# Kernel optimization log

Hardware: AMD Instinct MI355X
Metric: run time of the kernel (lower is better)

The kernel has to match this reference:

```python
import jax, jax.numpy as jnp
import numpy as np

B, S, NE = 4096, 128, 2
H = 64  # lstm hidden

def setup_inputs() -> dict:
    key = jax.random.key(0)
    ks = jax.random.split(key, 12)
    d = {
        'self_obs':     jax.random.normal(ks[0], (B, S, 15), jnp.float32),
        'teammate_obs': jax.random.normal(ks[1], (B, S, 13), jnp.float32),
        'enemy_obs':    jax.random.normal(ks[2], (B, S, NE, 13), jnp.float32),
        'next_cp_obs':  jax.random.normal(ks[3], (B, S, 6), jnp.float32),
        'W1':  jax.random.normal(ks[4], (47, 256), jnp.float32) * 0.1,
        'b1':  jnp.zeros((256,), jnp.float32),
        'W2':  jax.random.normal(ks[5], (256, 128), jnp.float32) * 0.1,
        'b2':  jnp.zeros((128,), jnp.float32),
        'Wih': jax.random.normal(ks[6], (128, 4 * H), jnp.float32) * 0.1,
        'bih': jnp.zeros((4 * H,), jnp.float32),
        'Whh': jax.random.normal(ks[7], (H, 4 * H), jnp.float32) * 0.1,
        'bhh': jnp.zeros((4 * H,), jnp.float32),
        'Wv':  jax.random.normal(ks[8], (H, 1), jnp.float32) * 0.1,
        'bv':  jnp.zeros((1,), jnp.float32),
    }
    return d

def reference(self_obs, teammate_obs, enemy_obs, next_cp_obs,
              W1, b1, W2, b2, Wih, bih, Whh, bhh, Wv, bv):
    # enemy pooling + concat -> [B,S,47]
    en_mean = enemy_obs.mean(axis=2)
    x = jnp.concatenate([self_obs, teammate_obs, en_mean, next_cp_obs], axis=2)
    # MLP encoder -> [B,S,128]
    emb = jax.nn.relu(jax.nn.relu(x @ W1 + b1) @ W2 + b2)
    # precompute input projection for all timesteps -> [B,S,4H]
    wx = emb @ Wih + bih
    h0 = jnp.zeros((B, H), wx.dtype)
    c0 = jnp.zeros((B, H), wx.dtype)

    def step(carry, wx_t):
        h, c = carry
        gates = wx_t + h @ Whh + bhh          # [B,4H]
        i, f, g, o = jnp.split(gates, 4, axis=-1)
        i = jax.nn.sigmoid(i)
        f = jax.nn.sigmoid(f)
        g = jnp.tanh(g)
        o = jax.nn.sigmoid(o)
        c = f * c + i * g
        h = o * jnp.tanh(c)
        return (h, c), h

    (hn, cn), outs = jax.lax.scan(step, (h0, c0), jnp.swapaxes(wx, 0, 1))
    out = jnp.swapaxes(outs, 0, 1)            # [B,S,H]
    val = (out @ Wv + bv).reshape(B, S, 1)
    return val, hn[None], cn[None]
```

## Files before the change

### kernel.cpp

```cpp
#include <hip/hip_runtime.h>
#include <hip/hip_bf16.h>

#define BB 4096
#define SS 128
#define NB 16
#define NT 256

typedef __attribute__((ext_vector_type(8))) short short8;
typedef __attribute__((ext_vector_type(4))) float f32x4;
typedef unsigned short ushort_t;
typedef unsigned int uint_t;

#define SX_STR   72
#define SH1_STR  264
#define SEMB_STR 136
#define SH_STR   72
#define ENC_LDS_USHORTS (64 * SH1_STR + 64 * SEMB_STR)

__device__ __forceinline__ ushort_t f2bf(float f) {
    union { __hip_bfloat16 b; ushort_t u; } x;
    x.b = __float2bfloat16(f);
    return x.u;
}
__device__ __forceinline__ uint_t pack2(float a, float b) {
    return (uint_t)f2bf(a) | ((uint_t)f2bf(b) << 16);
}
__device__ __forceinline__ float bflo(uint_t u) {
    union { unsigned u; float f; } x; x.u = u << 16; return x.f;
}
__device__ __forceinline__ float bfhi(uint_t u) {
    union { unsigned u; float f; } x; x.u = u & 0xFFFF0000u; return x.f;
}
__device__ __forceinline__ float bf2f(ushort_t h) {
    union { unsigned u; float f; } x; x.u = ((unsigned)h) << 16; return x.f;
}
__device__ __forceinline__ float fsig(float x) {
    return __builtin_amdgcn_rcpf(1.f + __expf(-x));
}
__device__ __forceinline__ float ftanh(float x) {
    return 1.f - 2.f * __builtin_amdgcn_rcpf(__expf(2.f * x) + 1.f);
}
__device__ __forceinline__ void barrier_lgkm() {
    asm volatile("s_waitcnt lgkmcnt(0)\n\ts_barrier" ::: "memory");
}

union FragU { short8 v; ushort_t u[8]; };

__global__ void podcritic_prep(const float* __restrict__ W1, const float* __restrict__ W2,
                               const float* __restrict__ Wih, const float* __restrict__ Whh,
                               short8* __restrict__ img)
{
    const int W = blockIdx.x * 4 + (threadIdx.x >> 6);
    const int l = threadIdx.x & 63;
    const int q = l >> 4, m = l & 15;
    FragU u;
    #pragma unroll
    for (int j = 0; j < 8; ++j) {
        float v;
        if (W < 32)       { int nt = W >> 1,        kk = W & 1;        int k = kk*32 + q*8 + j;
                            v = (k < 47) ? W1[k*256 + nt*16 + m] : 0.f; }
        else if (W < 96)  { int f = W - 32, nt = f >> 3, kk = f & 7;   int k = kk*32 + q*8 + j;
                            v = W2[k*128 + nt*16 + m]; }
        else if (W < 160) { int f = W - 96, nt = f >> 2, kk = f & 3;   int k = kk*32 + q*8 + j;
                            v = Wih[k*256 + nt*16 + m]; }
        else              { int f = W - 160, nt = f >> 1, kk = f & 1;  int k = kk*32 + q*8 + j;
                            v = Whh[k*256 + nt*16 + m]; }
        u.u[j] = f2bf(v);
    }
    img[W * 64 + l] = u.v;
}

__device__ __forceinline__ void enc_block(
    ushort_t* smem,
    const float* __restrict__ self_obs, const float* __restrict__ tm_obs,
    const float* __restrict__ en_obs,   const float* __restrict__ cp_obs,
    const float* __restrict__ b1, const float* __restrict__ b2,
    const float* __restrict__ bih, const float* __restrict__ bhh,
    const short8* __restrict__ img, uint_t* __restrict__ wx, int c0, int e)
{
    ushort_t* sh1 = smem;
    ushort_t* sxe = smem + 64 * SH1_STR;

    const int t = threadIdx.x;
    const int w = t >> 6, l = t & 63, q = l >> 4, m = l & 15;
    const int bg = e & 255, b0 = bg * NB;
    const int ytile = e >> 8;
    const int sbase = c0 + ytile * 4;

    {
        const int col = t & 63, rw0 = t >> 6;
        const float* p; int stride, soff; float scale;
        if (col < 15)      { p = self_obs + col;      stride = 15; soff = 0;  scale = 0.5f; }
        else if (col < 28) { p = tm_obs + (col - 15); stride = 13; soff = 0;  scale = 0.5f; }
        else if (col < 41) { p = en_obs + (col - 28); stride = 26; soff = 13; scale = 0.5f; }
        else if (col < 47) { p = cp_obs + (col - 41); stride = 6;  soff = 0;  scale = 0.5f; }
        else               { p = self_obs;            stride = 0;  soff = 0;  scale = 0.f; }
        #pragma unroll
        for (int jj = 0; jj < 16; ++jj) {
            int rr = 4 * jj + rw0;
            int mt = rr >> 4, r = rr & 15;
            int bs = (b0 + r) * SS + sbase + mt;
            int o = bs * stride;
            float v = scale * (p[o] + p[o + soff]);
            sxe[rr * SX_STR + col] = f2bf(v);
        }
    }
    float bias1[4], bias2[2], bgf[4];
    #pragma unroll
    for (int i = 0; i < 4; ++i) bias1[i] = b1[w * 64 + i * 16 + m];
    #pragma unroll
    for (int i = 0; i < 2; ++i) bias2[i] = b2[32 * w + 16 * i + m];
    #pragma unroll
    for (int i = 0; i < 4; ++i) { int n = (w + 4 * i) * 16 + m; bgf[i] = bih[n] + bhh[n]; }
    barrier_lgkm();

    {
        short8 w1f[4][2];
        #pragma unroll
        for (int i = 0; i < 4; ++i)
            #pragma unroll
            for (int kk = 0; kk < 2; ++kk)
                w1f[i][kk] = img[(((4 * w + i) * 2) + kk) * 64 + l];
        f32x4 c1[4][4];
        #pragma unroll
        for (int mt = 0; mt < 4; ++mt)
            #pragma unroll
            for (int i = 0; i < 4; ++i)
                c1[mt][i] = (f32x4){bias1[i], bias1[i], bias1[i], bias1[i]};
        #pragma unroll
        for (int kk = 0; kk < 2; ++kk) {
            #pragma unroll
            for (int mt = 0; mt < 4; ++mt) {
                short8 a = *(const short8*)&sxe[(mt * 16 + m) * SX_STR + kk * 32 + q * 8];
                #pragma unroll
                for (int i = 0; i < 4; ++i)
                    c1[mt][i] = __builtin_amdgcn_mfma_f32_16x16x32_bf16(a, w1f[i][kk], c1[mt][i], 0, 0, 0);
            }
        }
        #pragma unroll
        for (int mt = 0; mt < 4; ++mt)
            #pragma unroll
            for (int i = 0; i < 4; ++i) {
                int col = w * 64 + i * 16 + m;
                #pragma unroll
                for (int r = 0; r < 4; ++r)
                    sh1[(mt * 16 + q * 4 + r) * SH1_STR + col] = f2bf(fmaxf(c1[mt][i][r], 0.f));
            }
    }
    barrier_lgkm();

    {
        short8 w2f[2][8];
        #pragma unroll
        for (int i = 0; i < 2; ++i)
            #pragma unroll
            for (int kk = 0; kk < 8; ++kk)
                w2f[i][kk] = img[(32 + ((2 * w + i) * 8) + kk) * 64 + l];
        f32x4 c2[4][2];
        #pragma unroll
        for (int mt = 0; mt < 4; ++mt)
            #pragma unroll
            for (int i = 0; i < 2; ++i)
                c2[mt][i] = (f32x4){bias2[i], bias2[i], bias2[i], bias2[i]};
        #pragma unroll
        for (int kk = 0; kk < 8; ++kk) {
            #pragma unroll
            for (int mt = 0; mt < 4; ++mt) {
                short8 a = *(const short8*)&sh1[(mt * 16 + m) * SH1_STR + kk * 32 + q * 8];
                #pragma unroll
                for (int i = 0; i < 2; ++i)
                    c2[mt][i] = __builtin_amdgcn_mfma_f32_16x16x32_bf16(a, w2f[i][kk], c2[mt][i], 0, 0, 0);
            }
        }
        #pragma unroll
        for (int mt = 0; mt < 4; ++mt)
            #pragma unroll
            for (int i = 0; i < 2; ++i) {
                int col = 32 * w + 16 * i + m;
                #pragma unroll
                for (int r = 0; r < 4; ++r)
                    sxe[(mt * 16 + q * 4 + r) * SEMB_STR + col] = f2bf(fmaxf(c2[mt][i][r], 0.f));
            }
    }
    barrier_lgkm();

    {
        short8 wihf[4][4];
        #pragma unroll
        for (int i = 0; i < 4; ++i)
            #pragma unroll
            for (int kk = 0; kk < 4; ++kk)
                wihf[i][kk] = img[(96 + ((w + 4 * i) * 4) + kk) * 64 + l];
        #pragma unroll
        for (int mt = 0; mt < 4; ++mt) {
            f32x4 g[4];
            #pragma unroll
            for (int i = 0; i < 4; ++i) g[i] = (f32x4){bgf[i], bgf[i], bgf[i], bgf[i]};
            #pragma unroll
            for (int kk = 0; kk < 4; ++kk) {
                short8 a = *(const short8*)&sxe[(mt * 16 + m) * SEMB_STR + kk * 32 + q * 8];
                #pragma unroll
                for (int i = 0; i < 4; ++i)
                    g[i] = __builtin_amdgcn_mfma_f32_16x16x32_bf16(a, wihf[i][kk], g[i], 0, 0, 0);
            }
            int slc = ytile * 4 + mt;
            uint_t* dst = wx + (size_t)(slc * 256 + bg) * 2048 + l * 2;
            #pragma unroll
            for (int i = 0; i < 4; ++i) {
                uint2 vv;
                vv.x = pack2(g[i][0], g[i][1]);
                vv.y = pack2(g[i][2], g[i][3]);
                *(uint2*)(dst + (w + 4 * i) * 128) = vv;
            }
        }
    }
}

__device__ __forceinline__ void rec_block(
    ushort_t* smem,
    const short8* __restrict__ whhimg, const uint_t* __restrict__ wx,
    ushort_t* __restrict__ hws, float* __restrict__ cws,
    const float* __restrict__ Wv, const float* __restrict__ bv,
    float* __restrict__ out, int rc0, int first, int last, int csr)
{
    const int t = threadIdx.x;
    const int w = t >> 6, l = t & 63, q = l >> 4, m = l & 15;
    const int bg = blockIdx.x, b0 = bg * NB;
    const int vr = t >> 4, vp = t & 15;

    short8 whhf[4][2];
    #pragma unroll
    for (int a = 0; a < 4; ++a)
        #pragma unroll
        for (int kk = 0; kk < 2; ++kk)
            whhf[a][kk] = whhimg[(((w + 4 * a) * 2) + kk) * 64 + l];

    const float4 wv = *(const float4*)(Wv + vp * 4);
    const float bvv = bv[0];

    float creg[4], hlast[4] = {0.f, 0.f, 0.f, 0.f};
    if (first) {
        #pragma unroll
        for (int r = 0; r < 4; ++r) creg[r] = 0.f;
        int idx4 = t * 4, row = idx4 >> 6, col = idx4 & 63;
        uint2 z; z.x = 0u; z.y = 0u;
        *(uint2*)&smem[row * SH_STR + col] = z;
    } else {
        int idx4 = t * 4, row = idx4 >> 6, col = idx4 & 63;
        uint2 hv2 = *(const uint2*)((const uint_t*)(hws + (size_t)bg * 1024 + idx4));
        *(uint2*)&smem[row * SH_STR + col] = hv2;
        float4 cv = *(const float4*)(cws + ((size_t)bg * 256 + t) * 4);
        creg[0] = cv.x; creg[1] = cv.y; creg[2] = cv.z; creg[3] = cv.w;
    }

    uint2 upf[2][4];
    {
        const uint_t* p0 = wx + (size_t)(0 * 256 + bg) * 2048 + l * 2;
        const uint_t* p1 = wx + (size_t)(1 * 256 + bg) * 2048 + l * 2;
        #pragma unroll
        for (int a = 0; a < 4; ++a) {
            upf[0][a] = *(const uint2*)(p0 + (w + 4 * a) * 128);
            upf[1][a] = *(const uint2*)(p1 + (w + 4 * a) * 128);
        }
    }

    barrier_lgkm();

    #define REC_CORE(PAR, SLV)                                                          \
        const int sl_ = (SLV);                                                          \
        ushort_t* shc = smem + (PAR) * (NB * SH_STR);                                   \
        ushort_t* shn = smem + (1 - (PAR)) * (NB * SH_STR);                             \
        short8 af0 = *(const short8*)&shc[m * SH_STR + q * 8];                          \
        short8 af1 = *(const short8*)&shc[m * SH_STR + 32 + q * 8];                     \
        f32x4 g[4];                                                                     \
        _Pragma("unroll")                                                               \
        for (int a = 0; a < 4; ++a) {                                                   \
            g[a][0] = bflo(upf[PAR][a].x); g[a][1] = bfhi(upf[PAR][a].x);               \
            g[a][2] = bflo(upf[PAR][a].y); g[a][3] = bfhi(upf[PAR][a].y);               \
        }                                                                               \
        {                                                                               \
            int snext = (sl_ + 2 < csr) ? (sl_ + 2) : sl_;                              \
            const uint_t* pn = wx + (size_t)(snext * 256 + bg) * 2048 + l * 2;          \
            _Pragma("unroll")                                                           \
            for (int a = 0; a < 4; ++a)                                                 \
                upf[PAR][a] = *(const uint2*)(pn + (w + 4 * a) * 128);                  \
        }                                                                               \
        _Pragma("unroll")                                                               \
        for (int a = 0; a < 4; ++a) {                                                   \
            g[a] = __builtin_amdgcn_mfma_f32_16x16x32_bf16(af0, whhf[a][0], g[a], 0, 0, 0); \
            g[a] = __builtin_amdgcn_mfma_f32_16x16x32_bf16(af1, whhf[a][1], g[a], 0, 0, 0); \
        }                                                                               \
        _Pragma("unroll")                                                               \
        for (int r = 0; r < 4; ++r) {                                                   \
            float gi = fsig(g[0][r]);                                                   \
            float gf = fsig(g[1][r]);                                                   \
            float gg = ftanh(g[2][r]);                                                  \
            float go = fsig(g[3][r]);                                                   \
            float c  = gf * creg[r] + gi * gg;                                          \
            creg[r] = c;                                                                \
            float h = go * ftanh(c);                                                    \
            hlast[r] = h;                                                               \
            shn[(q * 4 + r) * SH_STR + 16 * w + m] = f2bf(h);                           \
        }

    for (int sl = 0; sl < csr; sl += 2) {
        {
            REC_CORE(0, sl);
            barrier_lgkm();
        }
        {
            uint2 hvA = *(const uint2*)&smem[1 * (NB * SH_STR) + vr * SH_STR + vp * 4];
            REC_CORE(1, sl + 1);
            barrier_lgkm();
            uint2 hvB = *(const uint2*)&shn[vr * SH_STR + vp * 4];
            float pvA = bflo(hvA.x) * wv.x + bfhi(hvA.x) * wv.y
                      + bflo(hvA.y) * wv.z + bfhi(hvA.y) * wv.w;
            float pvB = bflo(hvB.x) * wv.x + bfhi(hvB.x) * wv.y
                      + bflo(hvB.y) * wv.z + bfhi(hvB.y) * wv.w;
            pvA += __shfl_xor(pvA, 1, 16);  pvB += __shfl_xor(pvB, 1, 16);
            pvA += __shfl_xor(pvA, 2, 16);  pvB += __shfl_xor(pvB, 2, 16);
            pvA += __shfl_xor(pvA, 4, 16);  pvB += __shfl_xor(pvB, 4, 16);
            pvA += __shfl_xor(pvA, 8, 16);  pvB += __shfl_xor(pvB, 8, 16);
            if (vp == 0) {
                float2 o; o.x = pvA + bvv; o.y = pvB + bvv;
                *(float2*)&out[(size_t)(b0 + vr) * SS + rc0 + sl_ - 1] = o;
            }
        }
    }
    #undef REC_CORE

    if (!last) {
        const int jcol = 16 * w + m;
        #pragma unroll
        for (int r = 0; r < 4; ++r)
            hws[(size_t)bg * 1024 + (q * 4 + r) * 64 + jcol] = f2bf(hlast[r]);
        float4 cv; cv.x = creg[0]; cv.y = creg[1]; cv.z = creg[2]; cv.w = creg[3];
        *(float4*)(cws + ((size_t)bg * 256 + t) * 4) = cv;
    } else {
        const int jcol = 16 * w + m;
        #pragma unroll
        for (int r = 0; r < 4; ++r) {
            int row = b0 + q * 4 + r;
            out[BB * SS + (size_t)row * 64 + jcol]           = hlast[r];
            out[BB * SS + BB * 64 + (size_t)row * 64 + jcol] = creg[r];
        }
    }
}

__global__ __launch_bounds__(NT, 3)
void podcritic_step(const float* __restrict__ self_obs, const float* __restrict__ tm_obs,
                    const float* __restrict__ en_obs,   const float* __restrict__ cp_obs,
                    const float* __restrict__ b1, const float* __restrict__ b2,
                    const float* __restrict__ bih, const float* __restrict__ bhh,
                    const short8* __restrict__ img,
                    uint_t* __restrict__ wx_enc, const uint_t* __restrict__ wx_rec,
                    ushort_t* __restrict__ hws, float* __restrict__ cws,
                    const float* __restrict__ Wv, const float* __restrict__ bv,
                    float* __restrict__ out,
                    int enc_c0, int rec_c0, int nrec, int first, int last, int rec_cs)
{
    __shared__ __align__(16) ushort_t smem[ENC_LDS_USHORTS];
    const int bid = blockIdx.x;
    if (bid < nrec) {
        rec_block(smem, img + 160 * 64, wx_rec, hws, cws, Wv, bv, out,
                  rec_c0, first, last, rec_cs);
    } else {
        enc_block(smem, self_obs, tm_obs, en_obs, cp_obs, b1, b2, bih, bhh,
                  img, wx_enc, enc_c0, bid - nrec);
    }
}

__global__ __launch_bounds__(NT, 1)
void podcritic_mfma(const float* __restrict__ self_obs,
                    const float* __restrict__ tm_obs,
                    const float* __restrict__ en_obs,
                    const float* __restrict__ cp_obs,
                    const float* __restrict__ W1, const float* __restrict__ b1,
                    const float* __restrict__ W2, const float* __restrict__ b2,
                    const float* __restrict__ Wih, const float* __restrict__ bih,
                    const float* __restrict__ Whh, const float* __restrict__ bhh,
                    const float* __restrict__ Wv, const float* __restrict__ bv,
                    float* __restrict__ out)
{
    __shared__ __align__(16) ushort_t sx[2][NB * SX_STR];
    __shared__ __align__(16) ushort_t sh1[NB * SH1_STR];
    __shared__ __align__(16) ushort_t semb[NB * SEMB_STR];
    __shared__ __align__(16) ushort_t sh[NB * SH_STR];
    __shared__ float sWv[64];

    const int t  = threadIdx.x;
    const int w  = t >> 6;
    const int l  = t & 63;
    const int q  = l >> 4;
    const int m  = l & 15;
    const int b0 = blockIdx.x * NB;

    short8 w1f[4][2];
    short8 w2f[2][8];
    short8 wihf[4][4];
    short8 whhf[4][2];
    float bias1[4], bias2[2], bg[4];

    #pragma unroll
    for (int i = 0; i < 4; ++i) {
        int n = w * 64 + i * 16 + m;
        bias1[i] = b1[n];
        #pragma unroll
        for (int kk = 0; kk < 2; ++kk) {
            FragU u;
            #pragma unroll
            for (int j = 0; j < 8; ++j) {
                int k = kk * 32 + q * 8 + j;
                u.u[j] = f2bf(k < 47 ? W1[k * 256 + n] : 0.f);
            }
            w1f[i][kk] = u.v;
        }
    }
    #pragma unroll
    for (int i = 0; i < 2; ++i) {
        int n = 32 * w + i * 16 + m;
        bias2[i] = b2[n];
        #pragma unroll
        for (int kk = 0; kk < 8; ++kk) {
            FragU u;
            #pragma unroll
            for (int j = 0; j < 8; ++j) {
                int k = kk * 32 + q * 8 + j;
                u.u[j] = f2bf(W2[k * 128 + n]);
            }
            w2f[i][kk] = u.v;
        }
    }
    #pragma unroll
    for (int i = 0; i < 4; ++i) {
        int n = (w + 4 * i) * 16 + m;
        bg[i] = bih[n] + bhh[n];
        #pragma unroll
        for (int kk = 0; kk < 4; ++kk) {
            FragU u;
            #pragma unroll
            for (int j = 0; j < 8; ++j) {
                int k = kk * 32 + q * 8 + j;
                u.u[j] = f2bf(Wih[k * 256 + n]);
            }
            wihf[i][kk] = u.v;
        }
        #pragma unroll
        for (int kk = 0; kk < 2; ++kk) {
            FragU u;
            #pragma unroll
            for (int j = 0; j < 8; ++j) {
                int k = kk * 32 + q * 8 + j;
                u.u[j] = f2bf(Whh[k * 256 + n]);
            }
            whhf[i][kk] = u.v;
        }
    }
    const float bvv = bv[0];
    if (t < 64) sWv[t] = Wv[t];

    for (int idx = t; idx < NB * SH_STR; idx += NT) sh[idx] = 0;

    const int pcol = t & 63;
    const int prow = t >> 6;
    #pragma unroll
    for (int j = 0; j < 4; ++j) {
        int r  = 4 * j + prow;
        int bs = (b0 + r) * SS + 0;
        float v = 0.f;
        if (pcol < 15)      v = self_obs[bs * 15 + pcol];
        else if (pcol < 28) v = tm_obs[bs * 13 + (pcol - 15)];
        else if (pcol < 41) { int kk = pcol - 28;
                              v = 0.5f * (en_obs[(bs * 2) * 13 + kk] + en_obs[(bs * 2) * 13 + 13 + kk]); }
        else if (pcol < 47) v = cp_obs[bs * 6 + (pcol - 41)];
        sx[0][r * SX_STR + pcol] = f2bf(v);
    }
    __syncthreads();

    float creg[4] = {0.f, 0.f, 0.f, 0.f};
    float hreg[4] = {0.f, 0.f, 0.f, 0.f};
    int cur = 0;

    for (int s = 0; s < SS; ++s) {
        float pf[4];
        #pragma unroll
        for (int j = 0; j < 4; ++j) {
            float v = 0.f;
            if (s + 1 < SS) {
                int r  = 4 * j + prow;
                int bs = (b0 + r) * SS + (s + 1);
                if (pcol < 15)      v = self_obs[bs * 15 + pcol];
                else if (pcol < 28) v = tm_obs[bs * 13 + (pcol - 15)];
                else if (pcol < 41) { int kk = pcol - 28;
                                      v = 0.5f * (en_obs[(bs * 2) * 13 + kk] + en_obs[(bs * 2) * 13 + 13 + kk]); }
                else if (pcol < 47) v = cp_obs[bs * 6 + (pcol - 41)];
            }
            pf[j] = v;
        }

        {
            f32x4 c1[4] = {{0,0,0,0},{0,0,0,0},{0,0,0,0},{0,0,0,0}};
            #pragma unroll
            for (int kk = 0; kk < 2; ++kk) {
                short8 a = *(const short8*)&sx[cur][m * SX_STR + kk * 32 + q * 8];
                #pragma unroll
                for (int i = 0; i < 4; ++i)
                    c1[i] = __builtin_amdgcn_mfma_f32_16x16x32_bf16(a, w1f[i][kk], c1[i], 0, 0, 0);
            }
            #pragma unroll
            for (int i = 0; i < 4; ++i) {
                int col = w * 64 + i * 16 + m;
                #pragma unroll
                for (int r = 0; r < 4; ++r)
                    sh1[(q * 4 + r) * SH1_STR + col] = f2bf(fmaxf(c1[i][r] + bias1[i], 0.f));
            }
        }
        __syncthreads();

        {
            f32x4 c2[2] = {{0,0,0,0},{0,0,0,0}};
            #pragma unroll
            for (int kk = 0; kk < 8; ++kk) {
                short8 a = *(const short8*)&sh1[m * SH1_STR + kk * 32 + q * 8];
                #pragma unroll
                for (int i = 0; i < 2; ++i)
                    c2[i] = __builtin_amdgcn_mfma_f32_16x16x32_bf16(a, w2f[i][kk], c2[i], 0, 0, 0);
            }
            #pragma unroll
            for (int i = 0; i < 2; ++i) {
                int col = 32 * w + i * 16 + m;
                #pragma unroll
                for (int r = 0; r < 4; ++r)
                    semb[(q * 4 + r) * SEMB_STR + col] = f2bf(fmaxf(c2[i][r] + bias2[i], 0.f));
            }
        }
        __syncthreads();

        {
            f32x4 g[4];
            #pragma unroll
            for (int i = 0; i < 4; ++i) g[i] = (f32x4){bg[i], bg[i], bg[i], bg[i]};
            #pragma unroll
            for (int kk = 0; kk < 4; ++kk) {
                short8 a = *(const short8*)&semb[m * SEMB_STR + kk * 32 + q * 8];
                #pragma unroll
                for (int i = 0; i < 4; ++i)
                    g[i] = __builtin_amdgcn_mfma_f32_16x16x32_bf16(a, wihf[i][kk], g[i], 0, 0, 0);
            }
            #pragma unroll
            for (int kk = 0; kk < 2; ++kk) {
                short8 a = *(const short8*)&sh[m * SH_STR + kk * 32 + q * 8];
                #pragma unroll
                for (int i = 0; i < 4; ++i)
                    g[i] = __builtin_amdgcn_mfma_f32_16x16x32_bf16(a, whhf[i][kk], g[i], 0, 0, 0);
            }
            const int jcol = 16 * w + m;
            #pragma unroll
            for (int r = 0; r < 4; ++r) {
                float gi = fsig(g[0][r]);
                float gf = fsig(g[1][r]);
                float gg = ftanh(g[2][r]);
                float go = fsig(g[3][r]);
                float c  = gf * creg[r] + gi * gg;
                creg[r] = c;
                float h = go * ftanh(c);
                hreg[r] = h;
                sh[(q * 4 + r) * SH_STR + jcol] = f2bf(h);
            }
            #pragma unroll
            for (int j = 0; j < 4; ++j) {
                int r = 4 * j + prow;
                sx[cur ^ 1][r * SX_STR + pcol] = f2bf(pf[j]);
            }
        }
        __syncthreads();

        {
            int r = t >> 4, pp = t & 15;
            const ushort_t* hp = &sh[r * SH_STR + pp * 4];
            float pv = 0.f;
            #pragma unroll
            for (int j = 0; j < 4; ++j) pv += bf2f(hp[j]) * sWv[pp * 4 + j];
            pv += __shfl_xor(pv, 1, 16);
            pv += __shfl_xor(pv, 2, 16);
            pv += __shfl_xor(pv, 4, 16);
            pv += __shfl_xor(pv, 8, 16);
            if (pp == 0) out[(b0 + r) * SS + s] = pv + bvv;
        }
        cur ^= 1;
    }

    {
        const int jcol = 16 * w + m;
        #pragma unroll
        for (int r = 0; r < 4; ++r) {
            int row = b0 + q * 4 + r;
            out[BB * SS + row * 64 + jcol]           = hreg[r];
            out[BB * SS + BB * 64 + row * 64 + jcol] = creg[r];
        }
    }
}

extern "C" void kernel_launch(void* const* d_in, const int* in_sizes, int n_in,
                              void* d_out, int out_size, void* d_ws, size_t ws_size,
                              hipStream_t stream) {
    const float* self_obs = (const float*)d_in[0];
    const float* tm_obs   = (const float*)d_in[1];
    const float* en_obs   = (const float*)d_in[2];
    const float* cp_obs   = (const float*)d_in[3];
    const float* W1  = (const float*)d_in[4];
    const float* b1  = (const float*)d_in[5];
    const float* W2  = (const float*)d_in[6];
    const float* b2  = (const float*)d_in[7];
    const float* Wih = (const float*)d_in[8];
    const float* bih = (const float*)d_in[9];
    const float* Whh = (const float*)d_in[10];
    const float* bhh = (const float*)d_in[11];
    const float* Wv  = (const float*)d_in[12];
    const float* bv  = (const float*)d_in[13];
    float* out = (float*)d_out;

    const size_t h_bytes   = 256 * 1024 * 2;
    const size_t c_bytes   = 256 * 1024 * 4;
    const size_t img_bytes = 192 * 64 * 16;

    auto need_for = [&](int cs) -> size_t {
        size_t wx_chunk = (size_t)cs * 256 * 2048 * 4;
        return 2 * wx_chunk + h_bytes + c_bytes + img_bytes;
    };

    int chunks[10]; int nch = 0; int csmax = 0;
    if (ws_size >= need_for(32)) {
        csmax = 32; nch = 6;
        chunks[0] = 4; chunks[1] = 28; chunks[2] = 32;
        chunks[3] = 32; chunks[4] = 28; chunks[5] = 4;
    } else if (ws_size >= need_for(16)) {
        csmax = 16; nch = 10;
        chunks[0] = 4; chunks[1] = 12;
        for (int i = 2; i < 8; ++i) chunks[i] = 16;
        chunks[8] = 12; chunks[9] = 4;
    }

    if (csmax) {
        const size_t wx_chunk = (size_t)csmax * 256 * 2048 * 4;
        char* p = (char*)d_ws;
        uint_t*   wxb[2] = { (uint_t*)p, (uint_t*)(p + wx_chunk) };
        ushort_t* hws    = (ushort_t*)(p + 2 * wx_chunk);
        float*    cws    = (float*)(p + 2 * wx_chunk + h_bytes);
        short8*   img    = (short8*)(p + 2 * wx_chunk + h_bytes + c_bytes);

        int off[11]; off[0] = 0;
        for (int i = 0; i < nch; ++i) off[i + 1] = off[i] + chunks[i];

        podcritic_prep<<<48, NT, 0, stream>>>(W1, W2, Wih, Whh, img);

        podcritic_step<<<64 * chunks[0], NT, 0, stream>>>(
            self_obs, tm_obs, en_obs, cp_obs, b1, b2, bih, bhh, img,
            wxb[0], wxb[0], hws, cws, Wv, bv, out,
            0, 0, 0, 0, 0, chunks[0]);

        for (int i = 0; i < nch; ++i) {
            int nenc = (i + 1 < nch) ? 64 * chunks[i + 1] : 0;
            int grid = 256 + nenc;
            podcritic_step<<<grid, NT, 0, stream>>>(
                self_obs, tm_obs, en_obs, cp_obs, b1, b2, bih, bhh, img,
                wxb[(i + 1) & 1], wxb[i & 1], hws, cws, Wv, bv, out,
                off[i + 1], off[i],
                256, (i == 0) ? 1 : 0, (i == nch - 1) ? 1 : 0, chunks[i]);
        }
    } else {
        podcritic_mfma<<<BB / NB, NT, 0, stream>>>(
            self_obs, tm_obs, en_obs, cp_obs,
            W1, b1, W2, b2, Wih, bih, Whh, bhh, Wv, bv, out);
    }
}
```

Measured before the change: 364.2 us.

## Move input projection into recurrent blocks, stream bf16 embeddings instead of gates

```diff
diff --git a/kernel.cpp b/kernel.cpp
--- a/kernel.cpp
+++ b/kernel.cpp
@@ -15,7 +15,7 @@
 #define SH1_STR  264
 #define SEMB_STR 136
 #define SH_STR   72
-#define ENC_LDS_USHORTS (64 * SH1_STR + 64 * SEMB_STR)
+#define ENC_LDS_USHORTS (64 * SH1_STR + 64 * SX_STR)
 
 __device__ __forceinline__ ushort_t f2bf(float f) {
     union { __hip_bfloat16 b; ushort_t u; } x;
@@ -75,8 +75,7 @@
     const float* __restrict__ self_obs, const float* __restrict__ tm_obs,
     const float* __restrict__ en_obs,   const float* __restrict__ cp_obs,
     const float* __restrict__ b1, const float* __restrict__ b2,
-    const float* __restrict__ bih, const float* __restrict__ bhh,
-    const short8* __restrict__ img, uint_t* __restrict__ wx, int c0, int e)
+    const short8* __restrict__ img, ushort_t* __restrict__ ebuf, int c0, int e)
 {
     ushort_t* sh1 = smem;
     ushort_t* sxe = smem + 64 * SH1_STR;
@@ -105,13 +104,11 @@
             sxe[rr * SX_STR + col] = f2bf(v);
         }
     }
-    float bias1[4], bias2[2], bgf[4];
+    float bias1[4], bias2[2];
     #pragma unroll
     for (int i = 0; i < 4; ++i) bias1[i] = b1[w * 64 + i * 16 + m];
     #pragma unroll
     for (int i = 0; i < 2; ++i) bias2[i] = b2[32 * w + 16 * i + m];
-    #pragma unroll
-    for (int i = 0; i < 4; ++i) { int n = (w + 4 * i) * 16 + m; bgf[i] = bih[n] + bhh[n]; }
     barrier_lgkm();
 
     {
@@ -173,53 +170,25 @@
             }
         }
         #pragma unroll
-        for (int mt = 0; mt < 4; ++mt)
+        for (int mt = 0; mt < 4; ++mt) {
+            int slc = ytile * 4 + mt;
+            ushort_t* eb = ebuf + ((size_t)(slc * 256 + bg) * 16) * 128;
             #pragma unroll
             for (int i = 0; i < 2; ++i) {
                 int col = 32 * w + 16 * i + m;
                 #pragma unroll
                 for (int r = 0; r < 4; ++r)
-                    sxe[(mt * 16 + q * 4 + r) * SEMB_STR + col] = f2bf(fmaxf(c2[mt][i][r], 0.f));
-            }
-    }
-    barrier_lgkm();
-
-    {
-        short8 wihf[4][4];
-        #pragma unroll
-        for (int i = 0; i < 4; ++i)
-            #pragma unroll
-            for (int kk = 0; kk < 4; ++kk)
-                wihf[i][kk] = img[(96 + ((w + 4 * i) * 4) + kk) * 64 + l];
-        #pragma unroll
-        for (int mt = 0; mt < 4; ++mt) {
-            f32x4 g[4];
-            #pragma unroll
-            for (int i = 0; i < 4; ++i) g[i] = (f32x4){bgf[i], bgf[i], bgf[i], bgf[i]};
-            #pragma unroll
-            for (int kk = 0; kk < 4; ++kk) {
-                short8 a = *(const short8*)&sxe[(mt * 16 + m) * SEMB_STR + kk * 32 + q * 8];
-                #pragma unroll
-                for (int i = 0; i < 4; ++i)
-                    g[i] = __builtin_amdgcn_mfma_f32_16x16x32_bf16(a, wihf[i][kk], g[i], 0, 0, 0);
-            }
-            int slc = ytile * 4 + mt;
-            uint_t* dst = wx + (size_t)(slc * 256 + bg) * 2048 + l * 2;
-            #pragma unroll
-            for (int i = 0; i < 4; ++i) {
-                uint2 vv;
-                vv.x = pack2(g[i][0], g[i][1]);
-                vv.y = pack2(g[i][2], g[i][3]);
-                *(uint2*)(dst + (w + 4 * i) * 128) = vv;
+                    eb[(q * 4 + r) * 128 + col] = f2bf(fmaxf(c2[mt][i][r], 0.f));
             }
         }
     }
 }
 
 __device__ __forceinline__ void rec_block(
-    ushort_t* smem,
-    const short8* __restrict__ whhimg, const uint_t* __restrict__ wx,
+    ushort_t* smem, const short8* __restrict__ img,
+    const ushort_t* __restrict__ ebuf,
     ushort_t* __restrict__ hws, float* __restrict__ cws,
+    const float* __restrict__ bih, const float* __restrict__ bhh,
     const float* __restrict__ Wv, const float* __restrict__ bv,
     float* __restrict__ out, int rc0, int first, int last, int csr)
 {
@@ -228,12 +197,19 @@
     const int bg = blockIdx.x, b0 = bg * NB;
     const int vr = t >> 4, vp = t & 15;
 
-    short8 whhf[4][2];
-    #pragma unroll
-    for (int a = 0; a < 4; ++a)
+    short8 wihf[4][4], whhf[4][2];
+    float bgf[4];
+    #pragma unroll
+    for (int a = 0; a < 4; ++a) {
+        int n = (w + 4 * a) * 16 + m;
+        bgf[a] = bih[n] + bhh[n];
+        #pragma unroll
+        for (int kk = 0; kk < 4; ++kk)
+            wihf[a][kk] = img[(96 + ((w + 4 * a) * 4) + kk) * 64 + l];
         #pragma unroll
         for (int kk = 0; kk < 2; ++kk)
-            whhf[a][kk] = whhimg[(((w + 4 * a) * 2) + kk) * 64 + l];
+            whhf[a][kk] = img[(160 + ((w + 4 * a) * 2) + kk) * 64 + l];
+    }
 
     const float4 wv = *(const float4*)(Wv + vp * 4);
     const float bvv = bv[0];
@@ -253,15 +229,14 @@
         creg[0] = cv.x; creg[1] = cv.y; creg[2] = cv.z; creg[3] = cv.w;
     }
 
-    uint2 upf[2][4];
-    {
-        const uint_t* p0 = wx + (size_t)(0 * 256 + bg) * 2048 + l * 2;
-        const uint_t* p1 = wx + (size_t)(1 * 256 + bg) * 2048 + l * 2;
-        #pragma unroll
-        for (int a = 0; a < 4; ++a) {
-            upf[0][a] = *(const uint2*)(p0 + (w + 4 * a) * 128);
-            upf[1][a] = *(const uint2*)(p1 + (w + 4 * a) * 128);
-        }
+    const ushort_t* ebase = ebuf + ((size_t)bg * 16 + m) * 128 + q * 8;
+    const size_t estep = (size_t)256 * 16 * 128;
+
+    short8 ef[2][4];
+    #pragma unroll
+    for (int kk = 0; kk < 4; ++kk) {
+        ef[0][kk] = *(const short8*)(ebase + 0 * estep + kk * 32);
+        ef[1][kk] = *(const short8*)(ebase + 1 * estep + kk * 32);
     }
 
     barrier_lgkm();
@@ -274,16 +249,20 @@
         short8 af1 = *(const short8*)&shc[m * SH_STR + 32 + q * 8];                     \
         f32x4 g[4];                                                                     \
         _Pragma("unroll")                                                               \
-        for (int a = 0; a < 4; ++a) {                                                   \
-            g[a][0] = bflo(upf[PAR][a].x); g[a][1] = bfhi(upf[PAR][a].x);               \
-            g[a][2] = bflo(upf[PAR][a].y); g[a][3] = bfhi(upf[PAR][a].y);               \
+        for (int a = 0; a < 4; ++a)                                                     \
+            g[a] = (f32x4){bgf[a], bgf[a], bgf[a], bgf[a]};                             \
+        _Pragma("unroll")                                                               \
+        for (int kk = 0; kk < 4; ++kk) {                                                \
+            _Pragma("unroll")                                                           \
+            for (int a = 0; a < 4; ++a)                                                 \
+                g[a] = __builtin_amdgcn_mfma_f32_16x16x32_bf16(ef[PAR][kk], wihf[a][kk], g[a], 0, 0, 0); \
         }                                                                               \
         {                                                                               \
             int snext = (sl_ + 2 < csr) ? (sl_ + 2) : sl_;                              \
-            const uint_t* pn = wx + (size_t)(snext * 256 + bg) * 2048 + l * 2;          \
+            const ushort_t* en_ = ebase + (size_t)snext * estep;                        \
             _Pragma("unroll")                                                           \
-            for (int a = 0; a < 4; ++a)                                                 \
-                upf[PAR][a] = *(const uint2*)(pn + (w + 4 * a) * 128);                  \
+            for (int kk = 0; kk < 4; ++kk)                                              \
+                ef[PAR][kk] = *(const short8*)(en_ + kk * 32);                          \
         }                                                                               \
         _Pragma("unroll")                                                               \
         for (int a = 0; a < 4; ++a) {                                                   \
@@ -353,7 +332,7 @@
                     const float* __restrict__ b1, const float* __restrict__ b2,
                     const float* __restrict__ bih, const float* __restrict__ bhh,
                     const short8* __restrict__ img,
-                    uint_t* __restrict__ wx_enc, const uint_t* __restrict__ wx_rec,
+                    ushort_t* __restrict__ eb_enc, const ushort_t* __restrict__ eb_rec,
                     ushort_t* __restrict__ hws, float* __restrict__ cws,
                     const float* __restrict__ Wv, const float* __restrict__ bv,
                     float* __restrict__ out,
@@ -362,11 +341,11 @@
     __shared__ __align__(16) ushort_t smem[ENC_LDS_USHORTS];
     const int bid = blockIdx.x;
     if (bid < nrec) {
-        rec_block(smem, img + 160 * 64, wx_rec, hws, cws, Wv, bv, out,
+        rec_block(smem, img, eb_rec, hws, cws, bih, bhh, Wv, bv, out,
                   rec_c0, first, last, rec_cs);
     } else {
-        enc_block(smem, self_obs, tm_obs, en_obs, cp_obs, b1, b2, bih, bhh,
-                  img, wx_enc, enc_c0, bid - nrec);
+        enc_block(smem, self_obs, tm_obs, en_obs, cp_obs, b1, b2,
+                  img, eb_enc, enc_c0, bid - nrec);
     }
 }
 
@@ -625,8 +604,8 @@
     const size_t img_bytes = 192 * 64 * 16;
 
     auto need_for = [&](int cs) -> size_t {
-        size_t wx_chunk = (size_t)cs * 256 * 2048 * 4;
-        return 2 * wx_chunk + h_bytes + c_bytes + img_bytes;
+        size_t eb_chunk = (size_t)cs * 256 * 16 * 128 * 2;
+        return 2 * eb_chunk + h_bytes + c_bytes + img_bytes;
     };
 
     int chunks[10]; int nch = 0; int csmax = 0;
@@ -642,12 +621,12 @@
     }
 
     if (csmax) {
-        const size_t wx_chunk = (size_t)csmax * 256 * 2048 * 4;
+        const size_t eb_chunk = (size_t)csmax * 256 * 16 * 128 * 2;
         char* p = (char*)d_ws;
-        uint_t*   wxb[2] = { (uint_t*)p, (uint_t*)(p + wx_chunk) };
-        ushort_t* hws    = (ushort_t*)(p + 2 * wx_chunk);
-        float*    cws    = (float*)(p + 2 * wx_chunk + h_bytes);
-        short8*   img    = (short8*)(p + 2 * wx_chunk + h_bytes + c_bytes);
+        ushort_t* ebufb[2] = { (ushort_t*)p, (ushort_t*)(p + eb_chunk) };
+        ushort_t* hws      = (ushort_t*)(p + 2 * eb_chunk);
+        float*    cws      = (float*)(p + 2 * eb_chunk + h_bytes);
+        short8*   img      = (short8*)(p + 2 * eb_chunk + h_bytes + c_bytes);
 
         int off[11]; off[0] = 0;
         for (int i = 0; i < nch; ++i) off[i + 1] = off[i] + chunks[i];
@@ -656,7 +635,7 @@
 
         podcritic_step<<<64 * chunks[0], NT, 0, stream>>>(
             self_obs, tm_obs, en_obs, cp_obs, b1, b2, bih, bhh, img,
-            wxb[0], wxb[0], hws, cws, Wv, bv, out,
+            ebufb[0], ebufb[0], hws, cws, Wv, bv, out,
             0, 0, 0, 0, 0, chunks[0]);
 
         for (int i = 0; i < nch; ++i) {
@@ -664,7 +643,7 @@
             int grid = 256 + nenc;
             podcritic_step<<<grid, NT, 0, stream>>>(
                 self_obs, tm_obs, en_obs, cp_obs, b1, b2, bih, bhh, img,
-                wxb[(i + 1) & 1], wxb[i & 1], hws, cws, Wv, bv, out,
+                ebufb[(i + 1) & 1], ebufb[i & 1], hws, cws, Wv, bv, out,
                 off[i + 1], off[i],
                 256, (i == 0) ? 1 : 0, (i == nch - 1) ? 1 : 0, chunks[i]);
         }
```

Measured after the change: 649.3 us. 1.78x slower.
